# Kernel optimization log

Measured on AMD Instinct MI355X. Metric: run time of the kernel, lower is better.

## Reference

```python
import jax, jax.numpy as jnp
import numpy as np

# Config mirrors init_kwargs
B = 8            # batch_size
L = 1024         # new tokens per sequence (prefill)
BS = 16          # block_size
MAXB = 128       # max_blocks_per_seq = ceil(2048/16)
H = 8            # num_kv_heads
D = 128          # head_dim
NLAYERS = 2
TOTAL = B * MAXB * NLAYERS  # 2048 total blocks


def setup_inputs() -> dict:
    key = jax.random.key(0)
    k1, k2 = jax.random.split(key)
    return {
        "layer_idx": 0,
        "key_states": jax.random.normal(k1, (B * L, H, D), jnp.float32),
        "value_states": jax.random.normal(k2, (B * L, H, D), jnp.float32),
        "input_len": jnp.full((B,), L, jnp.int32),
        "cu_seqlens": (jnp.arange(B + 1, dtype=jnp.int32) * L),
        "k_cache": jnp.zeros((TOTAL, H, BS, D), jnp.float32),
        "v_cache": jnp.zeros((TOTAL, H, BS, D), jnp.float32),
        "block_tables": jnp.zeros((B, MAXB), jnp.int32),  # layer slice
        "seq_lens": jnp.zeros((B,), jnp.int32),           # layer slice
        "free_blocks": jnp.arange(TOTAL, dtype=jnp.int32),
    }


def reference(layer_idx, key_states, value_states, input_len, cu_seqlens,
              k_cache, v_cache, block_tables, seq_lens, free_blocks):
    # ---- block allocation (vectorized form of the per-sequence python loop) ----
    old_nb = (seq_lens + BS - 1) // BS                 # blocks already held
    new_nb = (seq_lens + input_len + BS - 1) // BS     # blocks needed
    alloc = new_nb - old_nb                            # per-seq new blocks
    cum = jnp.cumsum(alloc)                            # tail-pop order: seq i gets
    num_free = free_blocks.shape[0]                    # free_blocks[num_free-cum[i] : ...]
    start = num_free - cum                             # [B]
    slots = jnp.arange(MAXB, dtype=jnp.int32)[None, :]                  # [1, MAXB]
    valid = (slots >= old_nb[:, None]) & (slots < new_nb[:, None])      # [B, MAXB]
    free_idx = jnp.clip(start[:, None] + (slots - old_nb[:, None]), 0, num_free - 1)
    bt = jnp.where(valid, free_blocks[free_idx], block_tables)          # updated table

    # ---- scatter new K/V tokens into paged cache (store_paged_kv) ----
    # assumes uniform input_len == L (as built in setup_inputs)
    t = jnp.arange(L, dtype=jnp.int32)[None, :]        # [1, L]
    tok_idx = cu_seqlens[:B][:, None] + t              # [B, L] index into packed K/V
    pos = seq_lens[:, None] + t                        # absolute position in sequence
    blk = jnp.take_along_axis(bt, pos // BS, axis=1)   # [B, L] physical block id
    off = pos % BS                                     # [B, L] offset within block

    keys = key_states[tok_idx.ravel()]                 # [B*L, H, D]
    vals = value_states[tok_idx.ravel()]
    k_new = k_cache.at[blk.ravel(), :, off.ravel(), :].set(keys)
    v_new = v_cache.at[blk.ravel(), :, off.ravel(), :].set(vals)
    return jnp.stack([k_new, v_new])  # [2, TOTAL, H, BS, D]
```

## Files before the change

kernel.cpp:

```cpp
#include <hip/hip_runtime.h>

typedef float float4n __attribute__((ext_vector_type(4)));

constexpr int B     = 8;
constexpr int BS    = 16;
constexpr int MAXB  = 128;
constexpr int H     = 8;
constexpr int D     = 128;
constexpr int TOTAL = 2048;

constexpr int C4   = TOTAL * H * BS * D / 4;
constexpr int PB4  = H * BS * D / 4;
constexpr int PT4  = H * D / 4;
constexpr int PO4  = D / 4;

__global__ __launch_bounds__(256) void paged_kv_kernel(
        const float4n* __restrict__ key_states,
        const float4n* __restrict__ value_states,
        const float4n* __restrict__ k_cache,
        const float4n* __restrict__ v_cache,
        const int*     __restrict__ input_len,
        const int*     __restrict__ cu_seqlens,
        const int*     __restrict__ block_tables,
        const int*     __restrict__ seq_lens,
        const int*     __restrict__ free_blocks,
        float4n*       __restrict__ out) {
    const int myblk = blockIdx.x;
    const int tid   = threadIdx.x;

    __shared__ int s_found;
    if (tid == 0) s_found = -1;
    __syncthreads();

    int cum = 0;
    #pragma unroll
    for (int b = 0; b < B; ++b) {
        const int sl  = seq_lens[b];
        const int il  = input_len[b];
        const int onb = (sl + BS - 1) >> 4;
        const int nnb = (sl + il + BS - 1) >> 4;
        cum += nnb - onb;
        const int st  = TOTAL - cum;
        const int j0  = sl >> 4;
        for (int j = j0 + tid; j < nnb; j += 256) {
            int cand;
            if (j >= onb) {
                int fi = st + (j - onb);
                fi = min(max(fi, 0), TOTAL - 1);
                cand = free_blocks[fi];
            } else {
                cand = block_tables[b * MAXB + j];
            }
            if (cand == myblk) s_found = (b << 20) | j;
        }
    }
    __syncthreads();
    const int m = s_found;

    const int base4 = myblk * PB4;

    if (m < 0) {
        #pragma unroll 4
        for (int t = 0; t < PB4 / 256; ++t) {
            const int i4 = (t << 8) + tid;
            float4n k = __builtin_nontemporal_load(&k_cache[base4 + i4]);
            float4n v = __builtin_nontemporal_load(&v_cache[base4 + i4]);
            __builtin_nontemporal_store(k, &out[base4 + i4]);
            __builtin_nontemporal_store(v, &out[C4 + base4 + i4]);
        }
    } else {
        const int b  = m >> 20;
        const int j  = m & 0xFFFFF;
        const int sl = seq_lens[b];
        const int il = input_len[b];
        const int cu = cu_seqlens[b];
        #pragma unroll 4
        for (int t = 0; t < PB4 / 256; ++t) {
            const int i4  = (t << 8) + tid;
            const int h   = i4 >> 9;
            const int off = (i4 >> 5) & 15;
            const int d4  = i4 & 31;
            const int pos = j * BS + off;
            float4n k, v;
            if (pos >= sl && pos < sl + il) {
                const int tok = cu + (pos - sl);
                const int si  = tok * PT4 + h * PO4 + d4;
                k = __builtin_nontemporal_load(&key_states[si]);
                v = __builtin_nontemporal_load(&value_states[si]);
            } else {
                k = __builtin_nontemporal_load(&k_cache[base4 + i4]);
                v = __builtin_nontemporal_load(&v_cache[base4 + i4]);
            }
            __builtin_nontemporal_store(k, &out[base4 + i4]);
            __builtin_nontemporal_store(v, &out[C4 + base4 + i4]);
        }
    }
}

extern "C" void kernel_launch(void* const* d_in, const int* in_sizes, int n_in,
                              void* d_out, int out_size, void* d_ws, size_t ws_size,
                              hipStream_t stream) {
    const float* key_states   = (const float*)d_in[1];
    const float* value_states = (const float*)d_in[2];
    const int*   input_len    = (const int*)d_in[3];
    const int*   cu_seqlens   = (const int*)d_in[4];
    const float* k_cache      = (const float*)d_in[5];
    const float* v_cache      = (const float*)d_in[6];
    const int*   block_tables = (const int*)d_in[7];
    const int*   seq_lens     = (const int*)d_in[8];
    const int*   free_blocks  = (const int*)d_in[9];

    paged_kv_kernel<<<TOTAL, 256, 0, stream>>>(
        (const float4n*)key_states, (const float4n*)value_states,
        (const float4n*)k_cache, (const float4n*)v_cache,
        input_len, cu_seqlens, block_tables, seq_lens, free_blocks,
        (float4n*)d_out);
}
```

Baseline: 475.9 us.

## Split into bulk cache memcpy plus per-slot scatter kernel

Replaces the single fused kernel, where each physical block searched the allocation to decide between copying old cache and writing new tokens, with two device-to-device memcpys of k_cache and v_cache into the output followed by a scatter kernel launched per (sequence, slot). This removes the per-block search and lets the driver copy engine or blit path handle the bulk copy. In exchange, the blocks that receive new tokens are written twice (once by the memcpy, once by the scatter), and the work now needs three stream operations instead of one launch.

```diff
diff --git a/kernel.cpp b/kernel.cpp
--- a/kernel.cpp
+++ b/kernel.cpp
@@ -9,88 +9,63 @@
 constexpr int D     = 128;
 constexpr int TOTAL = 2048;
 
-constexpr int C4   = TOTAL * H * BS * D / 4;
+constexpr int CE   = TOTAL * H * BS * D;
+constexpr int C4   = CE / 4;
 constexpr int PB4  = H * BS * D / 4;
 constexpr int PT4  = H * D / 4;
 constexpr int PO4  = D / 4;
 
-__global__ __launch_bounds__(256) void paged_kv_kernel(
+__global__ __launch_bounds__(256) void scatter_new_tokens(
         const float4n* __restrict__ key_states,
         const float4n* __restrict__ value_states,
-        const float4n* __restrict__ k_cache,
-        const float4n* __restrict__ v_cache,
         const int*     __restrict__ input_len,
         const int*     __restrict__ cu_seqlens,
         const int*     __restrict__ block_tables,
         const int*     __restrict__ seq_lens,
         const int*     __restrict__ free_blocks,
         float4n*       __restrict__ out) {
-    const int myblk = blockIdx.x;
-    const int tid   = threadIdx.x;
+    const int b = blockIdx.x >> 7;
+    const int j = blockIdx.x & (MAXB - 1);
+    const int tid = threadIdx.x;
 
-    __shared__ int s_found;
-    if (tid == 0) s_found = -1;
-    __syncthreads();
+    int cum = 0, st = 0, onb = 0, nnb = 0;
+    #pragma unroll
+    for (int bb = 0; bb <= b; ++bb) {
+        const int sl = seq_lens[bb];
+        onb = (sl + BS - 1) >> 4;
+        nnb = (sl + input_len[bb] + BS - 1) >> 4;
+        cum += nnb - onb;
+        st = TOTAL - cum;
+    }
+    const int sl = seq_lens[b];
+    const int il = input_len[b];
+    const int j0 = sl >> 4;
+    if (j < j0 || j >= nnb) return;
 
-    int cum = 0;
-    #pragma unroll
-    for (int b = 0; b < B; ++b) {
-        const int sl  = seq_lens[b];
-        const int il  = input_len[b];
-        const int onb = (sl + BS - 1) >> 4;
-        const int nnb = (sl + il + BS - 1) >> 4;
-        cum += nnb - onb;
-        const int st  = TOTAL - cum;
-        const int j0  = sl >> 4;
-        for (int j = j0 + tid; j < nnb; j += 256) {
-            int cand;
-            if (j >= onb) {
-                int fi = st + (j - onb);
-                fi = min(max(fi, 0), TOTAL - 1);
-                cand = free_blocks[fi];
-            } else {
-                cand = block_tables[b * MAXB + j];
-            }
-            if (cand == myblk) s_found = (b << 20) | j;
-        }
+    int blk;
+    if (j >= onb) {
+        int fi = st + (j - onb);
+        fi = min(max(fi, 0), TOTAL - 1);
+        blk = free_blocks[fi];
+    } else {
+        blk = block_tables[b * MAXB + j];
     }
-    __syncthreads();
-    const int m = s_found;
 
-    const int base4 = myblk * PB4;
+    const int cu    = cu_seqlens[b];
+    const int base4 = blk * PB4;
 
-    if (m < 0) {
-        #pragma unroll 4
-        for (int t = 0; t < PB4 / 256; ++t) {
-            const int i4 = (t << 8) + tid;
-            float4n k = __builtin_nontemporal_load(&k_cache[base4 + i4]);
-            float4n v = __builtin_nontemporal_load(&v_cache[base4 + i4]);
-            __builtin_nontemporal_store(k, &out[base4 + i4]);
-            __builtin_nontemporal_store(v, &out[C4 + base4 + i4]);
-        }
-    } else {
-        const int b  = m >> 20;
-        const int j  = m & 0xFFFFF;
-        const int sl = seq_lens[b];
-        const int il = input_len[b];
-        const int cu = cu_seqlens[b];
-        #pragma unroll 4
-        for (int t = 0; t < PB4 / 256; ++t) {
-            const int i4  = (t << 8) + tid;
-            const int h   = i4 >> 9;
-            const int off = (i4 >> 5) & 15;
-            const int d4  = i4 & 31;
-            const int pos = j * BS + off;
-            float4n k, v;
-            if (pos >= sl && pos < sl + il) {
-                const int tok = cu + (pos - sl);
-                const int si  = tok * PT4 + h * PO4 + d4;
-                k = __builtin_nontemporal_load(&key_states[si]);
-                v = __builtin_nontemporal_load(&value_states[si]);
-            } else {
-                k = __builtin_nontemporal_load(&k_cache[base4 + i4]);
-                v = __builtin_nontemporal_load(&v_cache[base4 + i4]);
-            }
+    #pragma unroll 4
+    for (int t = 0; t < PB4 / 256; ++t) {
+        const int i4  = (t << 8) + tid;
+        const int h   = i4 >> 9;
+        const int off = (i4 >> 5) & 15;
+        const int d4  = i4 & 31;
+        const int pos = j * BS + off;
+        if (pos >= sl && pos < sl + il) {
+            const int tok = cu + (pos - sl);
+            const int si  = tok * PT4 + h * PO4 + d4;
+            float4n k = __builtin_nontemporal_load(&key_states[si]);
+            float4n v = __builtin_nontemporal_load(&value_states[si]);
             __builtin_nontemporal_store(k, &out[base4 + i4]);
             __builtin_nontemporal_store(v, &out[C4 + base4 + i4]);
         }
@@ -110,9 +85,15 @@
     const int*   seq_lens     = (const int*)d_in[8];
     const int*   free_blocks  = (const int*)d_in[9];
 
-    paged_kv_kernel<<<TOTAL, 256, 0, stream>>>(
+    float* out = (float*)d_out;
+
+    hipMemcpyAsync(out,      k_cache, (size_t)CE * sizeof(float),
+                   hipMemcpyDeviceToDevice, stream);
+    hipMemcpyAsync(out + CE, v_cache, (size_t)CE * sizeof(float),
+                   hipMemcpyDeviceToDevice, stream);
+
+    scatter_new_tokens<<<B * MAXB, 256, 0, stream>>>(
         (const float4n*)key_states, (const float4n*)value_states,
-        (const float4n*)k_cache, (const float4n*)v_cache,
         input_len, cu_seqlens, block_tables, seq_lens, free_blocks,
-        (float4n*)d_out);
+        (float4n*)out);
 }
```

After: 499.1 us. +4.9%, slower.
